# Kernel tuning notes

Measured on AMD Instinct MI355X. Metric: run time of the kernel, lower is better.

Reference implementation:

```python
import jax, jax.numpy as jnp
import numpy as np
import math

L = 2; B = 128; CIN = 64; E = 64; H = 8; Wd = 8; NH = 8; MEM = 40
HD = E // NH; HW = H * Wd; THD = HD * HW  # 512
MASK_B = 3.0; NEG = -1e9; EPS = 1e-5


def _conv(x, w, b):
    y = jax.lax.conv_general_dilated(x, w, (1, 1), 'SAME',
                                     dimension_numbers=('NCHW', 'OIHW', 'NCHW'))
    return y + b[None, :, None, None]


def setup_inputs() -> dict:
    key = jax.random.key(0)
    ks = jax.random.split(key, 12)
    f = jax.random.normal
    return {
        'x': f(ks[0], (B, CIN, H, Wd), jnp.float32),
        'h0': f(ks[1], (L, B, E, H, Wd), jnp.float32),
        'c0': f(ks[2], (L, B, E, H, Wd), jnp.float32),
        'k0': f(ks[3], (L, B, NH, MEM, THD), jnp.float32),
        'v0': f(ks[4], (L, B, NH, MEM, THD), jnp.float32),
        'src_mask': jax.random.randint(ks[5], (B, MEM), 0, 2).astype(bool),
        'notdone': jnp.ones((B,), bool),
        'main_w': f(ks[6], (L, 5 * E, CIN + 2 * E, 3, 3), jnp.float32) * 0.05,
        'main_b': jnp.zeros((L, 5 * E), jnp.float32),
        'proj_w': f(ks[7], (L, 3 * E, CIN + E, 3, 3), jnp.float32) * 0.05,
        'proj_b': jnp.zeros((L, 3 * E), jnp.float32),
        'out_w': f(ks[8], (L, E, E, 3, 3), jnp.float32) * 0.05,
        'out_b': jnp.zeros((L, E), jnp.float32),
        'ln_w': jnp.ones((L, E, H, Wd), jnp.float32),
        'ln_b': jnp.zeros((L, E, H, Wd), jnp.float32),
        'pos_w': f(ks[9], (L, MEM, HW * E), jnp.float32) * 0.05,
        'pos_b': f(ks[10], (L, MEM, NH), jnp.float32) * 0.05,
    }


def reference(x, h0, c0, k0, v0, src_mask, notdone,
              main_w, main_b, proj_w, proj_b, out_w, out_b,
              ln_w, ln_b, pos_w, pos_b):
    nd = notdone.astype(x.dtype)[:, None, None, None]
    # rolling attention mask: reset finished episodes, shift left, open last slot
    m = src_mask | (~notdone)[:, None]
    m = jnp.concatenate([m[:, 1:], jnp.zeros((B, 1), bool)], axis=1)
    bias = jnp.where(m, NEG, 0.0).astype(x.dtype)        # (B, MEM)
    bias = bias.at[:, -1].set(MASK_B)
    out = h0[L - 1] * nd
    for n in range(L):
        inp = jnp.concatenate([x, out], axis=1)          # (B, CIN+E, H, W)
        h_cur = h0[n] * nd
        c_cur = c0[n] * nd
        gates = _conv(jnp.concatenate([inp, h_cur], axis=1), main_w[n], main_b[n])
        cc_i, cc_f, cc_o, cc_g, cc_a = jnp.split(gates, 5, axis=1)
        i = jax.nn.sigmoid(cc_i)
        fg = jax.nn.sigmoid(cc_f)
        o = jax.nn.sigmoid(cc_o)
        g = jnp.tanh(cc_g)
        a = jax.nn.sigmoid(cc_a)
        c_next = fg * c_cur + i * g
        # attention over rolling memory (mem_n slots of flattened spatial features)
        kqv = _conv(inp, proj_w[n], proj_b[n]).reshape(B, NH, 3 * HD, HW)
        k = kqv[:, :, :HD].reshape(B, NH, THD)
        q = kqv[:, :, HD:2 * HD].reshape(B, NH, THD) / math.sqrt(THD)
        v = kqv[:, :, 2 * HD:].reshape(B, NH, THD)
        pw = pos_w[n].reshape(MEM, NH, THD).transpose(1, 0, 2)  # (NH, MEM, THD)
        k_cat = jnp.concatenate([k0[n][:, :, 1:], k[:, :, None, :]], axis=2) + pw[None]
        v_cat = jnp.concatenate([v0[n][:, :, 1:], v[:, :, None, :]], axis=2)
        scores = (jnp.einsum('bnd,bnmd->bnm', q, k_cat)
                  + bias[:, None, :] + pos_b[n].T[None])
        attn_w = jax.nn.softmax(scores, axis=-1)
        attn = jnp.einsum('bnm,bnmd->bnd', attn_w, v_cat).reshape(B, E, H, Wd)
        ao = _conv(attn, out_w[n], out_b[n]) + inp[:, :E]
        mu = ao.mean(axis=(1, 2, 3), keepdims=True)
        var = ((ao - mu) ** 2).mean(axis=(1, 2, 3), keepdims=True)
        ao = (ao - mu) * jax.lax.rsqrt(var + EPS) * ln_w[n][None] + ln_b[n][None]
        c_next = c_next + a * jnp.tanh(ao)
        out = o * jnp.tanh(c_next)
    return out
```

## Files before the change

kernel.cpp:

```cpp
#include <hip/hip_runtime.h>
#include <hip/hip_bf16.h>

typedef __hip_bfloat16 bf16;
typedef unsigned short u16;
typedef __attribute__((ext_vector_type(8))) short short8;
typedef __attribute__((ext_vector_type(4))) float f32x4;

#define Bb   128
#define MEMm 40

__device__ __forceinline__ float LD(const void* p, size_t i, int f32) {
    return f32 ? ((const float*)p)[i] : __bfloat162float(((const bf16*)p)[i]);
}
__device__ __forceinline__ float S2F(short s) {
    u16 u = (u16)s;
    return __bfloat162float(*(bf16*)&u);
}
__device__ __forceinline__ int LDB(const void* p, int i, int isbyte) {
    return isbyte ? (int)((const unsigned char*)p)[i] : ((const int*)p)[i];
}
__device__ __forceinline__ void SPLIT(float v, u16& hi, u16& lo) {
    bf16 h = __float2bfloat16(v);
    float r = v - __bfloat162float(h);
    bf16 l = __float2bfloat16(r);
    hi = *(u16*)&h; lo = *(u16*)&l;
}

__global__ void detect_kernel(const void* __restrict__ x,
                              const void* __restrict__ src_mask,
                              const void* __restrict__ notdone,
                              int* __restrict__ flags) {
    __shared__ int s[3];
    const int t = threadIdx.x;
    if (t < 3) s[t] = 0;
    __syncthreads();
    const bf16* xb = (const bf16*)x;
    int bad = 0;
    for (int i = t; i < 4096; i += 256) {
        float v = __bfloat162float(xb[2 * i]);
        if (!(fabsf(v) < 1e4f)) bad = 1;
    }
    if (bad) atomicOr(&s[0], 1);
    int mb = 0;
    const unsigned* mi = (const unsigned*)src_mask;
    for (int i = t; i < 1280; i += 256) if (mi[i] > 1u) mb = 1;
    if (mb) atomicOr(&s[1], 1);
    int nb = 0;
    const unsigned* ni = (const unsigned*)notdone;
    for (int i = t; i < 32; i += 256) if (ni[i] > 1u) nb = 1;
    if (nb) atomicOr(&s[2], 1);
    __syncthreads();
    if (t < 3) flags[t] = s[t];
}

__global__ void setup_kernel(const void* __restrict__ src_mask,
                             const void* __restrict__ notdone,
                             const void* __restrict__ h0,
                             const void* __restrict__ mw,
                             const void* __restrict__ pw,
                             const void* __restrict__ ow,
                             const int* __restrict__ flags,
                             float* __restrict__ biasb,
                             float* __restrict__ outb, size_t hoff,
                             u16* __restrict__ whi, u16* __restrict__ wlo) {
    const int bid = blockIdx.x, t = threadIdx.x;
    const int isf32 = flags[0], mbyte = flags[1], ndbyte = flags[2];
    if (bid < 20) {
        int idx = bid * 256 + t;
        if (idx >= Bb * MEMm) return;
        int b = idx / MEMm, m = idx - b * MEMm;
        float v;
        if (m == MEMm - 1) v = 3.0f;
        else {
            bool masked = (LDB(src_mask, b * MEMm + m + 1, mbyte) != 0) ||
                          (LDB(notdone, b, ndbyte) == 0);
            v = masked ? -1e9f : 0.f;
        }
        biasb[idx] = v;
    } else if (bid < 276) {
        int idx = (bid - 20) * 256 + t;
        int b = idx >> 9;
        float nd = (LDB(notdone, b, ndbyte) != 0) ? 1.f : 0.f;
        size_t e = (size_t)idx * 8;
        float v[8];
        if (isf32) {
            const float* hp = (const float*)h0 + hoff + e;
            f32x4 a = *(const f32x4*)hp, c = *(const f32x4*)(hp + 4);
#pragma unroll
            for (int j = 0; j < 4; ++j) { v[j] = a[j]; v[4 + j] = c[j]; }
        } else {
            short8 s = *(const short8*)((const bf16*)h0 + hoff + e);
#pragma unroll
            for (int j = 0; j < 8; ++j) v[j] = S2F(s[j]);
        }
#pragma unroll
        for (int j = 0; j < 8; ++j) outb[e + j] = v[j] * nd;
    } else {
        int gi = (bid - 276) * 256 + t;
        if (gi >= 1622016) return;
        int layer = (gi >= 811008) ? 1 : 0;
        int i = gi - layer * 811008;
        float v;
        if (i < 552960) {
            int tap = i / 61440, r = i - tap * 61440, co = r / 192, ci = r - co * 192;
            v = LD(mw, (size_t)layer * 552960 + ((size_t)co * 192 + ci) * 9 + tap, isf32);
        } else if (i < 774144) {
            int j = i - 552960;
            int tap = j / 24576, r = j - tap * 24576, co = r / 128, ci = r - co * 128;
            v = LD(pw, (size_t)layer * 221184 + ((size_t)co * 128 + ci) * 9 + tap, isf32);
        } else {
            int j = i - 774144;
            int tap = j / 4096, r = j - tap * 4096, co = r / 64, ci = r - co * 64;
            v = LD(ow, (size_t)layer * 36864 + ((size_t)co * 64 + ci) * 9 + tap, isf32);
        }
        u16 h, l; SPLIT(v, h, l);
        whi[gi] = h; wlo[gi] = l;
    }
}

__global__ __launch_bounds__(256) void build_cin_t_kernel(
    const void* __restrict__ x, const float* __restrict__ prev_out,
    const void* __restrict__ h0, const void* __restrict__ notdone,
    const int* __restrict__ flags,
    u16* __restrict__ cin_hi, u16* __restrict__ cin_lo, size_t hoff) {
    __shared__ float sb[192 * 65];
    const int t = threadIdx.x, b = blockIdx.x;
    const int isf32 = flags[0], ndbyte = flags[2];
    float nd = (LDB(notdone, b, ndbyte) != 0) ? 1.f : 0.f;
    for (int i = t; i < 12288; i += 256) {
        int c = i >> 6, px = i & 63;
        float v;
        if (c < 64)       v = LD(x, (size_t)b * 4096 + i, isf32);
        else if (c < 128) v = prev_out[(size_t)b * 4096 + i - 4096];
        else              v = LD(h0, hoff + (size_t)b * 4096 + i - 8192, isf32) * nd;
        sb[c * 65 + px] = v;
    }
    __syncthreads();
    size_t base = (size_t)b * 12288;
    for (int i = t; i < 12288; i += 256) {
        int px = i / 192, c = i - px * 192;
        float v = sb[c * 65 + px];
        u16 h, l; SPLIT(v, h, l);
        cin_hi[base + i] = h; cin_lo[base + i] = l;
    }
}

struct ConvArgs {
    const u16 *Ahi, *Alo;
    const u16 *WhiA, *WloA, *WhiB, *WloB;
    const void *biasA, *biasB;
    float *OutA, *OutB;
    long long boffA, boffB;
    int Astr, KciA, KciB, CoutA, CoutB, ntA, NT;
};

__global__ __launch_bounds__(256) void conv_mfma_kernel(ConvArgs g,
                                                        const int* __restrict__ flags) {
    __shared__ __align__(16) u16 Alds[2][2][2600];
    __shared__ __align__(16) u16 Wlds[2][2][2560];
    const int t = threadIdx.x, w = t >> 6, lane = t & 63;
    const int bpair = w >> 1, half = w & 1;
    const int bx = blockIdx.x;
    const int nt = bx % g.NT, mblk = bx / g.NT;
    const bool isA = (nt < g.ntA);
    const u16* Whi = isA ? g.WhiA : g.WhiB;
    const u16* Wlo = isA ? g.WloA : g.WloB;
    const int Kci  = isA ? g.KciA : g.KciB;
    const int CoutT= isA ? g.CoutA : g.CoutB;
    float* Out     = isA ? g.OutA : g.OutB;
    const void* bias = isA ? g.biasA : g.biasB;
    const long long boff = isA ? g.boffA : g.boffB;
    const int n0 = (isA ? nt : nt - g.ntA) * 64;
    const int b = mblk * 2 + bpair;
    const int NITER = (Kci >> 5) * 9;
    const int isf32 = flags[0];

    if (half == 0 && lane < 40) { Alds[bpair][0][2560 + lane] = 0; Alds[bpair][1][2560 + lane] = 0; }

    f32x4 acc[4][2];
#pragma unroll
    for (int i = 0; i < 4; ++i)
#pragma unroll
        for (int j = 0; j < 2; ++j) { f32x4 z = {0.f, 0.f, 0.f, 0.f}; acc[i][j] = z; }

    const int co_l = t >> 2, jj = t & 3;
    uint4 hv, lv;
    auto issueW = [&](int it) {
        int kc = it / 9, tap = it - kc * 9;
        size_t o = ((size_t)(tap * CoutT + n0 + co_l)) * Kci + kc * 32 + jj * 8;
        hv = *(const uint4*)(Whi + o);
        lv = *(const uint4*)(Wlo + o);
    };

    issueW(0);
    for (int it = 0; it < NITER; ++it) {
        const int kc = it / 9, tap = it - kc * 9;
        const int par = it & 1;
        *(uint4*)&Wlds[par][0][co_l * 40 + jj * 8] = hv;
        *(uint4*)&Wlds[par][1][co_l * 40 + jj * 8] = lv;
        __syncthreads();
        if (it + 1 < NITER) issueW(it + 1);
        if (tap == 0) {
            int arow = half * 32 + (lane >> 1);
            int chalf = (lane & 1) * 16;
            size_t o = ((size_t)b * 64 + arow) * g.Astr + kc * 32 + chalf;
            const uint4* sh = (const uint4*)(g.Ahi + o);
            const uint4* sl = (const uint4*)(g.Alo + o);
            uint4 a0 = sh[0], a1 = sh[1];
            uint4 c0 = sl[0], c1 = sl[1];
            *(uint4*)&Alds[bpair][0][arow * 40 + chalf + 0] = a0;
            *(uint4*)&Alds[bpair][0][arow * 40 + chalf + 8] = a1;
            *(uint4*)&Alds[bpair][1][arow * 40 + chalf + 0] = c0;
            *(uint4*)&Alds[bpair][1][arow * 40 + chalf + 8] = c1;
            __syncthreads();
        }
        const int dy = tap / 3 - 1, dx = tap % 3 - 1;
        const int q8 = (lane >> 4) * 8;
        const int ml = lane & 15;
        short8 aH[4], aL[4];
#pragma unroll
        for (int mt = 0; mt < 4; ++mt) {
            int px = mt * 16 + ml;
            int yy = (px >> 3) + dy, xx = (px & 7) + dx;
            int row = ((unsigned)yy < 8u && (unsigned)xx < 8u) ? yy * 8 + xx : 64;
            int o = row * 40 + q8;
            aH[mt] = *(const short8*)&Alds[bpair][0][o];
            aL[mt] = *(const short8*)&Alds[bpair][1][o];
        }
#pragma unroll
        for (int nn = 0; nn < 2; ++nn) {
            int o = (half * 32 + nn * 16 + ml) * 40 + q8;
            short8 bH = *(const short8*)&Wlds[par][0][o];
            short8 bL = *(const short8*)&Wlds[par][1][o];
#pragma unroll
            for (int mt = 0; mt < 4; ++mt) {
                acc[mt][nn] = __builtin_amdgcn_mfma_f32_16x16x32_bf16(aH[mt], bH, acc[mt][nn], 0, 0, 0);
                acc[mt][nn] = __builtin_amdgcn_mfma_f32_16x16x32_bf16(aH[mt], bL, acc[mt][nn], 0, 0, 0);
                acc[mt][nn] = __builtin_amdgcn_mfma_f32_16x16x32_bf16(aL[mt], bH, acc[mt][nn], 0, 0, 0);
            }
        }
    }
    const int q = lane >> 4, ml = lane & 15;
#pragma unroll
    for (int nn = 0; nn < 2; ++nn) {
        int co = n0 + half * 32 + nn * 16 + ml;
        float bv = LD(bias, (size_t)boff + co, isf32);
#pragma unroll
        for (int mt = 0; mt < 4; ++mt) {
            f32x4 v = acc[mt][nn];
            v[0] += bv; v[1] += bv; v[2] += bv; v[3] += bv;
            *(f32x4*)&Out[((size_t)b * CoutT + co) * 64 + mt * 16 + q * 4] = v;
        }
    }
}

__global__ __launch_bounds__(256) void attn_kernel(
    const float* __restrict__ kqv,
    const void* __restrict__ k0,
    const void* __restrict__ v0,
    const void* __restrict__ pw,
    const void* __restrict__ pb,
    const float* __restrict__ biasb,
    const int* __restrict__ flags,
    u16* __restrict__ ahi, u16* __restrict__ alo,
    size_t kvoff, size_t pwoff, size_t pboff) {
    __shared__ float qv[512], kl[512], vl[512], sc[40], wexp[40];
    __shared__ float accbuf[4][512];
    const int t = threadIdx.x;
    const int isf32 = flags[0];
    const int b = blockIdx.x >> 3, h = blockIdx.x & 7;
    const size_t kqb = (size_t)b * 192 * 64;
    for (int d = t; d < 512; d += 256) {
        int hd = d >> 6, ss = d & 63;
        qv[d] = kqv[kqb + (h * 24 + 8 + hd) * 64 + ss] * 0.044194173824159216f;
        kl[d] = kqv[kqb + (h * 24 + 0 + hd) * 64 + ss];
        vl[d] = kqv[kqb + (h * 24 + 16 + hd) * 64 + ss];
    }
    __syncthreads();
    const int wid = t >> 6, lane = t & 63;
    const int d0 = lane * 8;
    const size_t kvbase = kvoff + ((size_t)(b * 8 + h)) * (size_t)(40 * 512);

    float q8[8];
#pragma unroll
    for (int j = 0; j < 8; ++j) q8[j] = qv[d0 + j];

    for (int m = wid; m < 40; m += 4) {
        float kc[8];
        if (m < 39) {
            if (isf32) {
                const float* kp = (const float*)k0 + kvbase + (size_t)(m + 1) * 512 + d0;
                f32x4 a = *(const f32x4*)kp, c = *(const f32x4*)(kp + 4);
#pragma unroll
                for (int j = 0; j < 4; ++j) { kc[j] = a[j]; kc[4 + j] = c[j]; }
            } else {
                short8 s = *(const short8*)((const bf16*)k0 + kvbase + (size_t)(m + 1) * 512 + d0);
#pragma unroll
                for (int j = 0; j < 8; ++j) kc[j] = S2F(s[j]);
            }
        } else {
#pragma unroll
            for (int j = 0; j < 8; ++j) kc[j] = kl[d0 + j];
        }
        if (isf32) {
            const float* pp = (const float*)pw + pwoff + (size_t)m * 4096 + h * 512 + d0;
            f32x4 a = *(const f32x4*)pp, c = *(const f32x4*)(pp + 4);
#pragma unroll
            for (int j = 0; j < 4; ++j) { kc[j] += a[j]; kc[4 + j] += c[j]; }
        } else {
            short8 s = *(const short8*)((const bf16*)pw + pwoff + (size_t)m * 4096 + h * 512 + d0);
#pragma unroll
            for (int j = 0; j < 8; ++j) kc[j] += S2F(s[j]);
        }
        float p = 0.f;
#pragma unroll
        for (int j = 0; j < 8; ++j) p += q8[j] * kc[j];
#pragma unroll
        for (int off = 32; off > 0; off >>= 1) p += __shfl_down(p, off, 64);
        if (lane == 0)
            sc[m] = p + biasb[b * 40 + m] + LD(pb, pboff + m * 8 + h, isf32);
    }
    __syncthreads();

    float mx = -1e30f;
    for (int m = 0; m < 40; ++m) mx = fmaxf(mx, sc[m]);
    if (t < 40) wexp[t] = __expf(sc[t] - mx);
    __syncthreads();
    float sum = 0.f;
    for (int m = 0; m < 40; ++m) sum += wexp[m];
    float rs = 1.f / sum;

    float acc8[8];
#pragma unroll
    for (int j = 0; j < 8; ++j) acc8[j] = 0.f;
    for (int m = wid; m < 40; m += 4) {
        float wgt = wexp[m];
        if (m < 39) {
            if (isf32) {
                const float* vp = (const float*)v0 + kvbase + (size_t)(m + 1) * 512 + d0;
                f32x4 a = *(const f32x4*)vp, c = *(const f32x4*)(vp + 4);
#pragma unroll
                for (int j = 0; j < 4; ++j) { acc8[j] += wgt * a[j]; acc8[4 + j] += wgt * c[j]; }
            } else {
                short8 s = *(const short8*)((const bf16*)v0 + kvbase + (size_t)(m + 1) * 512 + d0);
#pragma unroll
                for (int j = 0; j < 8; ++j) acc8[j] += wgt * S2F(s[j]);
            }
        } else {
#pragma unroll
            for (int j = 0; j < 8; ++j) acc8[j] += wgt * vl[d0 + j];
        }
    }
#pragma unroll
    for (int j = 0; j < 8; ++j) accbuf[wid][d0 + j] = acc8[j];
    __syncthreads();

    for (int d = t; d < 512; d += 256) {
        float acc = (accbuf[0][d] + accbuf[1][d]) + (accbuf[2][d] + accbuf[3][d]);
        acc *= rs;
        int ch = h * 8 + (d >> 6), px = d & 63;
        u16 hh, ll; SPLIT(acc, hh, ll);
        size_t o = (size_t)b * 4096 + px * 64 + ch;
        ahi[o] = hh; alo[o] = ll;
    }
}

__global__ __launch_bounds__(256) void ln_final_kernel(
    const float* __restrict__ convo,
    const void* __restrict__ x,
    const float* __restrict__ gates,
    const void* __restrict__ c0,
    const void* __restrict__ notdone,
    const void* __restrict__ lnw,
    const void* __restrict__ lnb,
    const int* __restrict__ flags,
    float* __restrict__ out_buf,
    void* __restrict__ dout, int write_out,
    size_t coff, size_t lnoff) {
    __shared__ float red[8];
    __shared__ float stats[2];
    const int t = threadIdx.x, b = blockIdx.x;
    const int isf32 = flags[0], ndbyte = flags[2];
    const size_t base = (size_t)b * 4096;
    float v[16];
    float sum = 0.f, sumsq = 0.f;
#pragma unroll
    for (int k = 0; k < 16; ++k) {
        int i = t + 256 * k;
        float val = convo[base + i] + LD(x, base + i, isf32);
        v[k] = val; sum += val; sumsq += val * val;
    }
#pragma unroll
    for (int off = 32; off > 0; off >>= 1) {
        sum   += __shfl_down(sum, off, 64);
        sumsq += __shfl_down(sumsq, off, 64);
    }
    const int wid = t >> 6, lane = t & 63;
    if (lane == 0) { red[wid] = sum; red[4 + wid] = sumsq; }
    __syncthreads();
    if (t == 0) {
        float ts = red[0] + red[1] + red[2] + red[3];
        float tq = red[4] + red[5] + red[6] + red[7];
        float mu = ts * (1.f / 4096.f);
        float var = tq * (1.f / 4096.f) - mu * mu;
        stats[0] = mu; stats[1] = rsqrtf(fmaxf(var, 0.f) + 1e-5f);
    }
    __syncthreads();
    float mu = stats[0], rstd = stats[1];
    float nd = (LDB(notdone, b, ndbyte) != 0) ? 1.f : 0.f;
    const size_t gbase = (size_t)b * 320 * 64;
#pragma unroll
    for (int k = 0; k < 16; ++k) {
        int i = t + 256 * k;
        int c = i >> 6, s = i & 63;
        float aon = (v[k] - mu) * rstd * LD(lnw, lnoff + i, isf32) + LD(lnb, lnoff + i, isf32);
        float gi = gates[gbase + (size_t)(c      ) * 64 + s];
        float gf = gates[gbase + (size_t)(c +  64) * 64 + s];
        float go = gates[gbase + (size_t)(c + 128) * 64 + s];
        float gg = gates[gbase + (size_t)(c + 192) * 64 + s];
        float ga = gates[gbase + (size_t)(c + 256) * 64 + s];
        gi = 1.f / (1.f + __expf(-gi));
        gf = 1.f / (1.f + __expf(-gf));
        go = 1.f / (1.f + __expf(-go));
        gg = tanhf(gg);
        ga = 1.f / (1.f + __expf(-ga));
        float cc = LD(c0, coff + base + i, isf32) * nd;
        float cn = gf * cc + gi * gg + ga * tanhf(aon);
        float o  = go * tanhf(cn);
        out_buf[base + i] = o;
        if (write_out) {
            if (isf32) ((float*)dout)[base + i] = o;
            else       ((bf16*)dout)[base + i] = __float2bfloat16(o);
        }
    }
}

extern "C" void kernel_launch(void* const* d_in, const int* in_sizes, int n_in,
                              void* d_out, int out_size, void* d_ws, size_t ws_size,
                              hipStream_t stream) {
    const void* x      = d_in[0];
    const void* h0     = d_in[1];
    const void* c0     = d_in[2];
    const void* k0     = d_in[3];
    const void* v0     = d_in[4];
    const void* src_mask = d_in[5];
    const void* notdone  = d_in[6];
    const void* main_w = d_in[7];
    const void* main_b = d_in[8];
    const void* proj_w = d_in[9];
    const void* proj_b = d_in[10];
    const void* out_w  = d_in[11];
    const void* out_b  = d_in[12];
    const void* ln_w   = d_in[13];
    const void* ln_b   = d_in[14];
    const void* pos_w  = d_in[15];
    const void* pos_b  = d_in[16];

    float* wsf = (float*)d_ws;
    int*   flags    = (int*)d_ws;
    float* bias_buf = wsf + 8;
    float* out_buf  = wsf + 8192;
    float* gates_buf= wsf + 532480;
    float* kqv_buf  = wsf + 3153920;
    u16* cin_hi     = (u16*)(wsf + 4726784);
    u16* cin_lo     = (u16*)(wsf + 5513216);
    float* convo_buf= wsf + 4726784;
    u16* attn_hi    = (u16*)(wsf + 5513216);
    u16* attn_lo    = (u16*)(wsf + 5775360);
    u16* wr_hi      = (u16*)(wsf + 6299648);
    u16* wr_lo      = (u16*)(wsf + 7110656);

    detect_kernel<<<1, 256, 0, stream>>>(x, src_mask, notdone, flags);
    setup_kernel<<<6612, 256, 0, stream>>>(src_mask, notdone, h0,
                                           main_w, proj_w, out_w, flags,
                                           bias_buf, out_buf, (size_t)524288,
                                           wr_hi, wr_lo);
    for (int n = 0; n < 2; ++n) {
        const size_t wb = (size_t)n * 811008;
        build_cin_t_kernel<<<128, 256, 0, stream>>>(x, out_buf, h0, notdone, flags,
                                                    cin_hi, cin_lo, (size_t)n * 524288);
        ConvArgs ga;
        ga.Ahi = cin_hi; ga.Alo = cin_lo; ga.Astr = 192;
        ga.WhiA = wr_hi + wb;          ga.WloA = wr_lo + wb;          ga.KciA = 192; ga.CoutA = 320;
        ga.WhiB = wr_hi + wb + 552960; ga.WloB = wr_lo + wb + 552960; ga.KciB = 128; ga.CoutB = 192;
        ga.biasA = main_b; ga.boffA = (long long)n * 320; ga.OutA = gates_buf;
        ga.biasB = proj_b; ga.boffB = (long long)n * 192; ga.OutB = kqv_buf;
        ga.ntA = 5; ga.NT = 8;
        conv_mfma_kernel<<<512, 256, 0, stream>>>(ga, flags);

        attn_kernel<<<1024, 256, 0, stream>>>(
            kqv_buf, k0, v0, pos_w, pos_b, bias_buf, flags, attn_hi, attn_lo,
            (size_t)n * 20971520, (size_t)n * 163840, (size_t)n * 320);

        ConvArgs oa;
        oa.Ahi = attn_hi; oa.Alo = attn_lo; oa.Astr = 64;
        oa.WhiA = wr_hi + wb + 774144; oa.WloA = wr_lo + wb + 774144; oa.KciA = 64; oa.CoutA = 64;
        oa.WhiB = oa.WhiA; oa.WloB = oa.WloA; oa.KciB = 64; oa.CoutB = 64;
        oa.biasA = out_b; oa.boffA = (long long)n * 64; oa.OutA = convo_buf;
        oa.biasB = out_b; oa.boffB = (long long)n * 64; oa.OutB = convo_buf;
        oa.ntA = 1; oa.NT = 1;
        conv_mfma_kernel<<<64, 256, 0, stream>>>(oa, flags);

        ln_final_kernel<<<128, 256, 0, stream>>>(
            convo_buf, x, gates_buf, c0, notdone, ln_w, ln_b, flags,
            out_buf, d_out, (n == 1) ? 1 : 0,
            (size_t)n * 524288, (size_t)n * 4096);
    }
}
```

Baseline: 614.2 us.

## Fuse input build into main conv and out-conv into LayerNorm/LSTM tail

Removes the build_cin_t kernel by having the main conv gather x, previous output and masked h0 directly from NCHW and split them to bf16 hi/lo while staging A tiles. It also merges the output projection conv with the LayerNorm and LSTM gate update into one per-batch tail kernel, so convo_buf no longer round-trips through memory. The block index mapping in the main conv is reordered so that consecutive blocks share a weight tile. The trade-offs are strided, non-vectorized A loads with redundant conversion inside the conv, and a tail kernel that runs only 128 blocks.

```diff
diff --git a/kernel.cpp b/kernel.cpp
--- a/kernel.cpp
+++ b/kernel.cpp
@@ -118,40 +118,14 @@
     }
 }
 
-__global__ __launch_bounds__(256) void build_cin_t_kernel(
-    const void* __restrict__ x, const float* __restrict__ prev_out,
-    const void* __restrict__ h0, const void* __restrict__ notdone,
-    const int* __restrict__ flags,
-    u16* __restrict__ cin_hi, u16* __restrict__ cin_lo, size_t hoff) {
-    __shared__ float sb[192 * 65];
-    const int t = threadIdx.x, b = blockIdx.x;
-    const int isf32 = flags[0], ndbyte = flags[2];
-    float nd = (LDB(notdone, b, ndbyte) != 0) ? 1.f : 0.f;
-    for (int i = t; i < 12288; i += 256) {
-        int c = i >> 6, px = i & 63;
-        float v;
-        if (c < 64)       v = LD(x, (size_t)b * 4096 + i, isf32);
-        else if (c < 128) v = prev_out[(size_t)b * 4096 + i - 4096];
-        else              v = LD(h0, hoff + (size_t)b * 4096 + i - 8192, isf32) * nd;
-        sb[c * 65 + px] = v;
-    }
-    __syncthreads();
-    size_t base = (size_t)b * 12288;
-    for (int i = t; i < 12288; i += 256) {
-        int px = i / 192, c = i - px * 192;
-        float v = sb[c * 65 + px];
-        u16 h, l; SPLIT(v, h, l);
-        cin_hi[base + i] = h; cin_lo[base + i] = l;
-    }
-}
-
 struct ConvArgs {
-    const u16 *Ahi, *Alo;
+    const void *x; const float *prev_out; const void *h0; const void *notdone;
     const u16 *WhiA, *WloA, *WhiB, *WloB;
     const void *biasA, *biasB;
     float *OutA, *OutB;
     long long boffA, boffB;
-    int Astr, KciA, KciB, CoutA, CoutB, ntA, NT;
+    size_t hoff;
+    int KciA, KciB, CoutA, CoutB, ntA, NT, NMB;
 };
 
 __global__ __launch_bounds__(256) void conv_mfma_kernel(ConvArgs g,
@@ -161,7 +135,7 @@
     const int t = threadIdx.x, w = t >> 6, lane = t & 63;
     const int bpair = w >> 1, half = w & 1;
     const int bx = blockIdx.x;
-    const int nt = bx % g.NT, mblk = bx / g.NT;
+    const int mblk = bx % g.NMB, nt = bx / g.NMB;
     const bool isA = (nt < g.ntA);
     const u16* Whi = isA ? g.WhiA : g.WhiB;
     const u16* Wlo = isA ? g.WloA : g.WloB;
@@ -174,6 +148,7 @@
     const int b = mblk * 2 + bpair;
     const int NITER = (Kci >> 5) * 9;
     const int isf32 = flags[0];
+    const float nd = (LDB(g.notdone, b, flags[2]) != 0) ? 1.f : 0.f;
 
     if (half == 0 && lane < 40) { Alds[bpair][0][2560 + lane] = 0; Alds[bpair][1][2560 + lane] = 0; }
 
@@ -201,17 +176,31 @@
         __syncthreads();
         if (it + 1 < NITER) issueW(it + 1);
         if (tap == 0) {
-            int arow = half * 32 + (lane >> 1);
-            int chalf = (lane & 1) * 16;
-            size_t o = ((size_t)b * 64 + arow) * g.Astr + kc * 32 + chalf;
-            const uint4* sh = (const uint4*)(g.Ahi + o);
-            const uint4* sl = (const uint4*)(g.Alo + o);
-            uint4 a0 = sh[0], a1 = sh[1];
-            uint4 c0 = sl[0], c1 = sl[1];
-            *(uint4*)&Alds[bpair][0][arow * 40 + chalf + 0] = a0;
-            *(uint4*)&Alds[bpair][0][arow * 40 + chalf + 8] = a1;
-            *(uint4*)&Alds[bpair][1][arow * 40 + chalf + 0] = c0;
-            *(uint4*)&Alds[bpair][1][arow * 40 + chalf + 8] = c1;
+            const int px = lane;
+            const int c0i = half * 16;
+            const int cbase = kc * 32;
+            short8 hA, hB, lA, lB;
+#pragma unroll
+            for (int cl2 = 0; cl2 < 16; ++cl2) {
+                int c = cbase + c0i + cl2;
+                float v;
+                if (c < 64) {
+                    size_t o = (size_t)b * 4096 + (size_t)c * 64 + px;
+                    v = isf32 ? ((const float*)g.x)[o] : S2F(((const short*)g.x)[o]);
+                } else if (c < 128) {
+                    v = g.prev_out[(size_t)b * 4096 + (size_t)(c - 64) * 64 + px];
+                } else {
+                    size_t o = g.hoff + (size_t)b * 4096 + (size_t)(c - 128) * 64 + px;
+                    v = (isf32 ? ((const float*)g.h0)[o] : S2F(((const short*)g.h0)[o])) * nd;
+                }
+                u16 hh, ll; SPLIT(v, hh, ll);
+                if (cl2 < 8) { hA[cl2] = (short)hh; lA[cl2] = (short)ll; }
+                else         { hB[cl2 - 8] = (short)hh; lB[cl2 - 8] = (short)ll; }
+            }
+            *(short8*)&Alds[bpair][0][px * 40 + c0i]     = hA;
+            *(short8*)&Alds[bpair][0][px * 40 + c0i + 8] = hB;
+            *(short8*)&Alds[bpair][1][px * 40 + c0i]     = lA;
+            *(short8*)&Alds[bpair][1][px * 40 + c0i + 8] = lB;
             __syncthreads();
         }
         const int dy = tap / 3 - 1, dx = tap % 3 - 1;
@@ -365,38 +354,104 @@
     }
 }
 
-__global__ __launch_bounds__(256) void ln_final_kernel(
-    const float* __restrict__ convo,
+__global__ __launch_bounds__(256) void tail_kernel(
+    const u16* __restrict__ ahi, const u16* __restrict__ alo,
+    const u16* __restrict__ whi, const u16* __restrict__ wlo,
+    const void* __restrict__ outb_bias,
     const void* __restrict__ x,
     const float* __restrict__ gates,
     const void* __restrict__ c0,
     const void* __restrict__ notdone,
-    const void* __restrict__ lnw,
-    const void* __restrict__ lnb,
+    const void* __restrict__ lnw, const void* __restrict__ lnb,
     const int* __restrict__ flags,
-    float* __restrict__ out_buf,
-    void* __restrict__ dout, int write_out,
-    size_t coff, size_t lnoff) {
-    __shared__ float red[8];
-    __shared__ float stats[2];
-    const int t = threadIdx.x, b = blockIdx.x;
+    float* __restrict__ out_buf, void* __restrict__ dout, int write_out,
+    long long boff, size_t coff, size_t lnoff) {
+    __shared__ __align__(16) u16 Ald[2][2][2600];
+    __shared__ __align__(16) u16 Wl[2][2][2560];
+    __shared__ float red[8], stats[2];
+    const int t = threadIdx.x, w = t >> 6, lane = t & 63;
+    const int b = blockIdx.x;
     const int isf32 = flags[0], ndbyte = flags[2];
+
+    {
+        int px = t >> 2, ci16 = (t & 3) * 16;
+        int chunk = ci16 >> 5, cl = ci16 & 31;
+        size_t o = ((size_t)b * 64 + px) * 64 + ci16;
+        *(uint4*)&Ald[chunk][0][px * 40 + cl]     = *(const uint4*)(ahi + o);
+        *(uint4*)&Ald[chunk][0][px * 40 + cl + 8] = *(const uint4*)(ahi + o + 8);
+        *(uint4*)&Ald[chunk][1][px * 40 + cl]     = *(const uint4*)(alo + o);
+        *(uint4*)&Ald[chunk][1][px * 40 + cl + 8] = *(const uint4*)(alo + o + 8);
+        if (t < 160) { int ch = t / 80, hl = (t / 40) & 1, i = t % 40;
+                       Ald[ch][hl][2560 + i] = 0; }
+    }
+
+    const int co_l = t >> 2, jj = t & 3;
+    uint4 hv, lv;
+    auto issueW = [&](int it) {
+        int kc = it / 9, tap = it - kc * 9;
+        size_t o = ((size_t)(tap * 64 + co_l)) * 64 + kc * 32 + jj * 8;
+        hv = *(const uint4*)(whi + o);
+        lv = *(const uint4*)(wlo + o);
+    };
+
+    f32x4 acc[4];
+#pragma unroll
+    for (int i = 0; i < 4; ++i) { f32x4 z = {0.f, 0.f, 0.f, 0.f}; acc[i] = z; }
+
+    issueW(0);
+    for (int it = 0; it < 18; ++it) {
+        const int kc = it / 9, tap = it - kc * 9;
+        const int par = it & 1;
+        *(uint4*)&Wl[par][0][co_l * 40 + jj * 8] = hv;
+        *(uint4*)&Wl[par][1][co_l * 40 + jj * 8] = lv;
+        __syncthreads();
+        if (it + 1 < 18) issueW(it + 1);
+        const int dy = tap / 3 - 1, dx = tap % 3 - 1;
+        const int q8 = (lane >> 4) * 8;
+        const int ml = lane & 15;
+        short8 aH[4], aL[4];
+#pragma unroll
+        for (int mt = 0; mt < 4; ++mt) {
+            int px = mt * 16 + ml;
+            int yy = (px >> 3) + dy, xx = (px & 7) + dx;
+            int row = ((unsigned)yy < 8u && (unsigned)xx < 8u) ? yy * 8 + xx : 64;
+            int o = row * 40 + q8;
+            aH[mt] = *(const short8*)&Ald[kc][0][o];
+            aL[mt] = *(const short8*)&Ald[kc][1][o];
+        }
+        int o = (w * 16 + ml) * 40 + q8;
+        short8 bH = *(const short8*)&Wl[par][0][o];
+        short8 bL = *(const short8*)&Wl[par][1][o];
+#pragma unroll
+        for (int mt = 0; mt < 4; ++mt) {
+            acc[mt] = __builtin_amdgcn_mfma_f32_16x16x32_bf16(aH[mt], bH, acc[mt], 0, 0, 0);
+            acc[mt] = __builtin_amdgcn_mfma_f32_16x16x32_bf16(aH[mt], bL, acc[mt], 0, 0, 0);
+            acc[mt] = __builtin_amdgcn_mfma_f32_16x16x32_bf16(aL[mt], bH, acc[mt], 0, 0, 0);
+        }
+    }
+
+    const int q = lane >> 4, ml = lane & 15;
+    const int co = w * 16 + ml;
     const size_t base = (size_t)b * 4096;
-    float v[16];
+    float bv = LD(outb_bias, (size_t)boff + co, isf32);
+    float vals[16];
     float sum = 0.f, sumsq = 0.f;
 #pragma unroll
-    for (int k = 0; k < 16; ++k) {
-        int i = t + 256 * k;
-        float val = convo[base + i] + LD(x, base + i, isf32);
-        v[k] = val; sum += val; sumsq += val * val;
+    for (int mt = 0; mt < 4; ++mt) {
+        int px0 = mt * 16 + q * 4;
+#pragma unroll
+        for (int r = 0; r < 4; ++r) {
+            float xv = LD(x, base + (size_t)co * 64 + px0 + r, isf32);
+            float val = acc[mt][r] + bv + xv;
+            vals[mt * 4 + r] = val; sum += val; sumsq += val * val;
+        }
     }
 #pragma unroll
     for (int off = 32; off > 0; off >>= 1) {
         sum   += __shfl_down(sum, off, 64);
         sumsq += __shfl_down(sumsq, off, 64);
     }
-    const int wid = t >> 6, lane = t & 63;
-    if (lane == 0) { red[wid] = sum; red[4 + wid] = sumsq; }
+    if (lane == 0) { red[w] = sum; red[4 + w] = sumsq; }
     __syncthreads();
     if (t == 0) {
         float ts = red[0] + red[1] + red[2] + red[3];
@@ -406,32 +461,39 @@
         stats[0] = mu; stats[1] = rsqrtf(fmaxf(var, 0.f) + 1e-5f);
     }
     __syncthreads();
-    float mu = stats[0], rstd = stats[1];
-    float nd = (LDB(notdone, b, ndbyte) != 0) ? 1.f : 0.f;
+    const float mu = stats[0], rstd = stats[1];
+    const float nd = (LDB(notdone, b, ndbyte) != 0) ? 1.f : 0.f;
     const size_t gbase = (size_t)b * 320 * 64;
 #pragma unroll
-    for (int k = 0; k < 16; ++k) {
-        int i = t + 256 * k;
-        int c = i >> 6, s = i & 63;
-        float aon = (v[k] - mu) * rstd * LD(lnw, lnoff + i, isf32) + LD(lnb, lnoff + i, isf32);
-        float gi = gates[gbase + (size_t)(c      ) * 64 + s];
-        float gf = gates[gbase + (size_t)(c +  64) * 64 + s];
-        float go = gates[gbase + (size_t)(c + 128) * 64 + s];
-        float gg = gates[gbase + (size_t)(c + 192) * 64 + s];
-        float ga = gates[gbase + (size_t)(c + 256) * 64 + s];
-        gi = 1.f / (1.f + __expf(-gi));
-        gf = 1.f / (1.f + __expf(-gf));
-        go = 1.f / (1.f + __expf(-go));
-        gg = tanhf(gg);
-        ga = 1.f / (1.f + __expf(-ga));
-        float cc = LD(c0, coff + base + i, isf32) * nd;
-        float cn = gf * cc + gi * gg + ga * tanhf(aon);
-        float o  = go * tanhf(cn);
-        out_buf[base + i] = o;
-        if (write_out) {
-            if (isf32) ((float*)dout)[base + i] = o;
-            else       ((bf16*)dout)[base + i] = __float2bfloat16(o);
-        }
+    for (int mt = 0; mt < 4; ++mt) {
+        int px0 = mt * 16 + q * 4;
+        size_t i0 = (size_t)co * 64 + px0;
+        f32x4 gi4 = *(const f32x4*)&gates[gbase + (size_t)(co      ) * 64 + px0];
+        f32x4 gf4 = *(const f32x4*)&gates[gbase + (size_t)(co +  64) * 64 + px0];
+        f32x4 go4 = *(const f32x4*)&gates[gbase + (size_t)(co + 128) * 64 + px0];
+        f32x4 gg4 = *(const f32x4*)&gates[gbase + (size_t)(co + 192) * 64 + px0];
+        f32x4 ga4 = *(const f32x4*)&gates[gbase + (size_t)(co + 256) * 64 + px0];
+        f32x4 ov;
+#pragma unroll
+        for (int r = 0; r < 4; ++r) {
+            size_t i = i0 + r;
+            float aon = (vals[mt * 4 + r] - mu) * rstd * LD(lnw, lnoff + i, isf32)
+                        + LD(lnb, lnoff + i, isf32);
+            float gi = 1.f / (1.f + __expf(-gi4[r]));
+            float gf = 1.f / (1.f + __expf(-gf4[r]));
+            float go = 1.f / (1.f + __expf(-go4[r]));
+            float gg = tanhf(gg4[r]);
+            float ga = 1.f / (1.f + __expf(-ga4[r]));
+            float cc = LD(c0, coff + base + i, isf32) * nd;
+            float cn = gf * cc + gi * gg + ga * tanhf(aon);
+            float o  = go * tanhf(cn);
+            ov[r] = o;
+            if (write_out) {
+                if (isf32) ((float*)dout)[base + i] = o;
+                else       ((bf16*)dout)[base + i] = __float2bfloat16(o);
+            }
+        }
+        *(f32x4*)&out_buf[base + i0] = ov;
     }
 }
 
@@ -462,13 +524,10 @@
     float* out_buf  = wsf + 8192;
     float* gates_buf= wsf + 532480;
     float* kqv_buf  = wsf + 3153920;
-    u16* cin_hi     = (u16*)(wsf + 4726784);
-    u16* cin_lo     = (u16*)(wsf + 5513216);
-    float* convo_buf= wsf + 4726784;
-    u16* attn_hi    = (u16*)(wsf + 5513216);
-    u16* attn_lo    = (u16*)(wsf + 5775360);
-    u16* wr_hi      = (u16*)(wsf + 6299648);
-    u16* wr_lo      = (u16*)(wsf + 7110656);
+    u16* attn_hi    = (u16*)(wsf + 4726784);
+    u16* attn_lo    = (u16*)(wsf + 4988928);
+    u16* wr_hi      = (u16*)(wsf + 5251072);
+    u16* wr_lo      = (u16*)(wsf + 6062080);
 
     detect_kernel<<<1, 256, 0, stream>>>(x, src_mask, notdone, flags);
     setup_kernel<<<6612, 256, 0, stream>>>(src_mask, notdone, h0,
@@ -477,33 +536,24 @@
                                            wr_hi, wr_lo);
     for (int n = 0; n < 2; ++n) {
         const size_t wb = (size_t)n * 811008;
-        build_cin_t_kernel<<<128, 256, 0, stream>>>(x, out_buf, h0, notdone, flags,
-                                                    cin_hi, cin_lo, (size_t)n * 524288);
         ConvArgs ga;
-        ga.Ahi = cin_hi; ga.Alo = cin_lo; ga.Astr = 192;
+        ga.x = x; ga.prev_out = out_buf; ga.h0 = h0; ga.notdone = notdone;
+        ga.hoff = (size_t)n * 524288;
         ga.WhiA = wr_hi + wb;          ga.WloA = wr_lo + wb;          ga.KciA = 192; ga.CoutA = 320;
         ga.WhiB = wr_hi + wb + 552960; ga.WloB = wr_lo + wb + 552960; ga.KciB = 128; ga.CoutB = 192;
         ga.biasA = main_b; ga.boffA = (long long)n * 320; ga.OutA = gates_buf;
         ga.biasB = proj_b; ga.boffB = (long long)n * 192; ga.OutB = kqv_buf;
-        ga.ntA = 5; ga.NT = 8;
+        ga.ntA = 5; ga.NT = 8; ga.NMB = 64;
         conv_mfma_kernel<<<512, 256, 0, stream>>>(ga, flags);
 
         attn_kernel<<<1024, 256, 0, stream>>>(
             kqv_buf, k0, v0, pos_w, pos_b, bias_buf, flags, attn_hi, attn_lo,
             (size_t)n * 20971520, (size_t)n * 163840, (size_t)n * 320);
 
-        ConvArgs oa;
-        oa.Ahi = attn_hi; oa.Alo = attn_lo; oa.Astr = 64;
-        oa.WhiA = wr_hi + wb + 774144; oa.WloA = wr_lo + wb + 774144; oa.KciA = 64; oa.CoutA = 64;
-        oa.WhiB = oa.WhiA; oa.WloB = oa.WloA; oa.KciB = 64; oa.CoutB = 64;
-        oa.biasA = out_b; oa.boffA = (long long)n * 64; oa.OutA = convo_buf;
-        oa.biasB = out_b; oa.boffB = (long long)n * 64; oa.OutB = convo_buf;
-        oa.ntA = 1; oa.NT = 1;
-        conv_mfma_kernel<<<64, 256, 0, stream>>>(oa, flags);
-
-        ln_final_kernel<<<128, 256, 0, stream>>>(
-            convo_buf, x, gates_buf, c0, notdone, ln_w, ln_b, flags,
+        tail_kernel<<<128, 256, 0, stream>>>(
+            attn_hi, attn_lo, wr_hi + wb + 774144, wr_lo + wb + 774144,
+            out_b, x, gates_buf, c0, notdone, ln_w, ln_b, flags,
             out_buf, d_out, (n == 1) ? 1 : 0,
-            (size_t)n * 524288, (size_t)n * 4096);
-    }
-}
+            (long long)n * 64, (size_t)n * 524288, (size_t)n * 4096);
+    }
+}
```

After: 572.5 us. 6.8% less time.
